# Kernel tuning notes

Hardware: AMD Instinct MI355X
Metric: run time of the kernel (lower is better)

Reference implementation:

```python
import jax, jax.numpy as jnp
import numpy as np

DT = 0.1
DX = 1.0
DY = 1.0
NUM_STEPS = 5
EPS = 1e-06


def _smooth3(c):
    # replicate-pad 3-tap mean filter along last axis (matches F.pad replicate + conv1d)
    cp = jnp.concatenate([c[..., :1], c, c[..., -1:]], axis=-1)
    return (cp[..., :-2] + cp[..., 1:-1] + cp[..., 2:]) / 3.0


def _thomas(a, b, c, d):
    # a, b, c, d: (M, N). Batched Thomas solve, sequential recurrence over N via lax.scan.
    M, N = d.shape
    a0 = a.at[:, 0].set(0.0)  # a[:,0] unused; zero it so the first scan step gives c0/(b0+eps)

    def fwd(carry, inp):
        c_prev, d_prev = carry
        ai, bi, ci, di = inp
        denom = bi - ai * c_prev + EPS
        cs = ci / denom
        ds = (di - ai * d_prev) / denom
        return (cs, ds), (cs, ds)

    init = (jnp.zeros((M,), d.dtype), jnp.zeros((M,), d.dtype))
    _, (c_star, d_star) = jax.lax.scan(fwd, init, (a0.T, b.T, c.T, d.T))  # (N, M)

    def bwd(x_next, inp):
        cs, ds = inp
        x = ds - cs * x_next
        return x, x

    x_last = d_star[-1]
    _, x_rest = jax.lax.scan(bwd, x_last, (c_star[:-1], d_star[:-1]), reverse=True)
    x = jnp.concatenate([x_rest, x_last[None, :]], axis=0)  # (N, M)
    return x.T


def _diffuse_rows(u2, coef2, dt, dh):
    # u2, coef2: (M, N) rows solved independently
    cs = _smooth3(coef2) * dt / (dh * dh)
    a = -cs
    c = -cs
    b = 1.0 + 2.0 * cs
    b = b.at[:, 0].set(1.0 + cs[:, 0])
    b = b.at[:, -1].set(1.0 + cs[:, -1])
    return _thomas(a, b, c, u2)


def _coef_at(base, tcoef, t):
    return jnp.clip(base + tcoef * t, EPS, None)


def _forward(u, alpha_base, beta_base, alpha_time_coeff, beta_time_coeff):
    B, C, H, W = u.shape
    t = 0.0
    for _ in range(NUM_STEPS):
        # half step in x
        alpha = _coef_at(alpha_base, alpha_time_coeff, t)  # (C,H,W)
        af = jnp.broadcast_to(alpha[None], (B, C, H, W)).reshape(B * C * H, W)
        u = _diffuse_rows(u.reshape(B * C * H, W), af, DT / 2, DX).reshape(B, C, H, W)
        t += DT / 2
        # full step in y (transpose H<->W)
        beta = _coef_at(beta_base, beta_time_coeff, t)
        ut = jnp.swapaxes(u, 2, 3).reshape(B * C * W, H)
        bf = jnp.broadcast_to(jnp.swapaxes(beta, 1, 2)[None], (B, C, W, H)).reshape(B * C * W, H)
        ut = _diffuse_rows(ut, bf, DT, DY).reshape(B, C, W, H)
        u = jnp.swapaxes(ut, 2, 3)
        t += DT / 2
        # half step in x
        alpha = _coef_at(alpha_base, alpha_time_coeff, t)
        af = jnp.broadcast_to(alpha[None], (B, C, H, W)).reshape(B * C * H, W)
        u = _diffuse_rows(u.reshape(B * C * H, W), af, DT / 2, DX).reshape(B, C, H, W)
    return u


def setup_inputs() -> dict:
    key = jax.random.key(0)
    k1, k2, k3, k4, k5 = jax.random.split(key, 5)
    B, C, S = 2048, 3, 32
    u = jax.random.normal(k1, (B, C, S, S), dtype=jnp.float32)
    alpha_base = 1.0 + 0.1 * jax.random.normal(k2, (C, S, S), dtype=jnp.float32)
    beta_base = 1.0 + 0.1 * jax.random.normal(k3, (C, S, S), dtype=jnp.float32)
    alpha_time_coeff = 0.05 * jax.random.normal(k4, (C, S, S), dtype=jnp.float32)
    beta_time_coeff = 0.05 * jax.random.normal(k5, (C, S, S), dtype=jnp.float32)
    return {"u": u, "alpha_base": alpha_base, "beta_base": beta_base,
            "alpha_time_coeff": alpha_time_coeff, "beta_time_coeff": beta_time_coeff}


def reference(u, alpha_base, beta_base, alpha_time_coeff, beta_time_coeff):
    return _forward(u, alpha_base, beta_base, alpha_time_coeff, beta_time_coeff)
```

## Files before the change

### kernel.cpp

```cpp
#include <hip/hip_runtime.h>

static constexpr float EPSF = 1e-6f;


__global__ __launch_bounds__(64) void coef_kernel(
    const float* __restrict__ alpha_base, const float* __restrict__ beta_base,
    const float* __restrict__ alpha_tc,   const float* __restrict__ beta_tc,
    float* __restrict__ pT, float* __restrict__ snT)
{
    int gid  = blockIdx.x * 64 + threadIdx.x;
    int pair = gid >> 5;
    int ln   = gid & 31;
    if (pair >= 33) return;
    int set = pair / 3;
    int ch  = pair % 3;
    bool isX = (set < 6);
    float t  = isX ? 0.1f * (float)set : 0.1f * (float)(set - 6) + 0.05f;
    float dt = isX ? 0.05f : 0.1f;

    const float* bp; const float* tp; int stride;
    if (isX) { bp = alpha_base + (ch * 32 + ln) * 32; tp = alpha_tc + (ch * 32 + ln) * 32; stride = 1; }
    else     { bp = beta_base  + ch * 1024 + ln;      tp = beta_tc  + ch * 1024 + ln;      stride = 32; }

    float c[32];
    #pragma unroll
    for (int i = 0; i < 32; ++i)
        c[i] = fmaxf(fmaf(tp[i * stride], t, bp[i * stride]), EPSF);

    float cs[32];
    #pragma unroll
    for (int i = 0; i < 32; ++i) {
        float l = (i == 0)  ? c[0]  : c[i - 1];
        float r = (i == 31) ? c[31] : c[i + 1];
        cs[i] = (l + c[i] + r) / 3.0f * dt;
    }

    float p[32], sn[32];
    {
        float den = (1.0f + cs[0]) + EPSF;
        p[0]  = 1.0f / den;
        sn[0] = cs[0] * p[0];
        float sprev = -sn[0];
        #pragma unroll
        for (int i = 1; i < 32; ++i) {
            float bi = (i == 31) ? (1.0f + cs[31]) : fmaf(2.0f, cs[i], 1.0f);
            float ai = -cs[i];
            float d  = (bi - ai * sprev) + EPSF;
            float pi = 1.0f / d;
            p[i]  = pi;
            float si = ai * pi;
            sn[i] = -si;
            sprev = si;
        }
    }

    float* po = pT  + (set * 3 + ch) * 1024 + ln;
    float* so = snT + (set * 3 + ch) * 1024 + ln;
    #pragma unroll
    for (int i = 0; i < 32; ++i) { po[i * 32] = p[i]; so[i * 32] = sn[i]; }
}

__device__ __forceinline__ void solve_ln(float d[32],
                                         const float* __restrict__ pb,
                                         const float* __restrict__ sb)
{
    float sn[32];
    #pragma unroll
    for (int i = 0; i < 32; ++i) sn[i] = sb[i * 32];

    float prev = d[0] * pb[0];
    d[0] = prev;
    #pragma unroll
    for (int i = 1; i < 32; ++i) {
        prev = fmaf(sn[i], prev, d[i] * pb[i * 32]);
        d[i] = prev;
    }
    #pragma unroll
    for (int i = 30; i >= 0; --i)
        d[i] = fmaf(sn[i], d[i + 1], d[i]);
}

__global__ __launch_bounds__(256, 3) void diff_kernel(
    const float* __restrict__ u_in, float* __restrict__ u_out,
    const float* __restrict__ pT, const float* __restrict__ snT,
    int blocksPerCh)
{
    __shared__ float tile[8 * 1056];
    const int tid = threadIdx.x;
    const int bid = blockIdx.x;
    const int ch  = bid / blocksPerCh;
    const int b0  = (bid % blocksPerCh) * 8;

    {
        const int r  = tid >> 3;
        const int c4 = (tid & 7) << 2;
        #pragma unroll
        for (int it = 0; it < 8; ++it) {
            const int slab = (b0 + it) * 3 + ch;
            const float4 v = reinterpret_cast<const float4*>(u_in + slab * 1024)[tid];
            float* dst = &tile[it * 1056 + r * 33 + c4];
            dst[0] = v.x; dst[1] = v.y; dst[2] = v.z; dst[3] = v.w;
        }
    }
    __syncthreads();

    const int ls = tid >> 5;
    const int ln = tid & 31;
    float* tb = &tile[ls * 1056];
    const float* pB = pT  + ch * 1024 + ln;
    const float* sB = snT + ch * 1024 + ln;

    float d[32];
    #pragma unroll
    for (int i = 0; i < 32; ++i) d[i] = tb[ln * 33 + i];

    solve_ln(d, pB, sB);

    for (int step = 0; step < 5; ++step) {
        #pragma unroll
        for (int i = 0; i < 32; ++i) tb[ln * 33 + i] = d[i];
        __syncthreads();
        #pragma unroll
        for (int i = 0; i < 32; ++i) d[i] = tb[i * 33 + ln];
        {
            const int off = (6 + step) * 3072;
            solve_ln(d, pB + off, sB + off);
        }
        #pragma unroll
        for (int i = 0; i < 32; ++i) tb[i * 33 + ln] = d[i];
        __syncthreads();
        #pragma unroll
        for (int i = 0; i < 32; ++i) d[i] = tb[ln * 33 + i];

        {
            const int off = (step + 1) * 3072;
            solve_ln(d, pB + off, sB + off);
            if (step < 4) solve_ln(d, pB + off, sB + off);
        }
    }

    #pragma unroll
    for (int i = 0; i < 32; ++i) tb[ln * 33 + i] = d[i];
    __syncthreads();
    {
        const int r  = tid >> 3;
        const int c4 = (tid & 7) << 2;
        #pragma unroll
        for (int it = 0; it < 8; ++it) {
            const int slab = (b0 + it) * 3 + ch;
            const float* s_ = &tile[it * 1056 + r * 33 + c4];
            float4 v; v.x = s_[0]; v.y = s_[1]; v.z = s_[2]; v.w = s_[3];
            reinterpret_cast<float4*>(u_out + slab * 1024)[tid] = v;
        }
    }
}

extern "C" void kernel_launch(void* const* d_in, const int* in_sizes, int n_in,
                              void* d_out, int out_size, void* d_ws, size_t ws_size,
                              hipStream_t stream)
{
    const float* u   = (const float*)d_in[0];
    const float* ab  = (const float*)d_in[1];
    const float* bb  = (const float*)d_in[2];
    const float* atc = (const float*)d_in[3];
    const float* btc = (const float*)d_in[4];
    float* out = (float*)d_out;
    float* pT  = (float*)d_ws;
    float* snT = pT + 33 * 1024;

    const int B = in_sizes[0] / (3 * 32 * 32);
    const int blocksPerCh = B / 8;

    coef_kernel<<<17, 64, 0, stream>>>(ab, bb, atc, btc, pT, snT);
    diff_kernel<<<3 * blocksPerCh, 256, 0, stream>>>(u, out, pT, snT, blocksPerCh);
}
```

Before: 115.9 us.

## Make each wavefront own two slabs, drop barriers, interleave coefficients as float2

The u tile load and store are remapped so each 64-lane wavefront handles exactly the two 32x32 slabs it later solves, which lets all __syncthreads be removed. Coefficient tables are interleaved into float2 and loaded into registers ahead of each sweep, with sched_barrier to prefetch during LDS traffic. Row padding changes from 33 to 34 so rows can be read and written with float2 LDS accesses. The costs are higher register pressure from holding 64 coefficient values per lane, and reliance on wavefront-local LDS ordering instead of block barriers.

```diff
diff --git a/kernel.cpp b/kernel.cpp
--- a/kernel.cpp
+++ b/kernel.cpp
@@ -6,7 +6,7 @@
 __global__ __launch_bounds__(64) void coef_kernel(
     const float* __restrict__ alpha_base, const float* __restrict__ beta_base,
     const float* __restrict__ alpha_tc,   const float* __restrict__ beta_tc,
-    float* __restrict__ pT, float* __restrict__ snT)
+    float2* __restrict__ C2)
 {
     int gid  = blockIdx.x * 64 + threadIdx.x;
     int pair = gid >> 5;
@@ -45,8 +45,8 @@
         for (int i = 1; i < 32; ++i) {
             float bi = (i == 31) ? (1.0f + cs[31]) : fmaf(2.0f, cs[i], 1.0f);
             float ai = -cs[i];
-            float d  = (bi - ai * sprev) + EPSF;
-            float pi = 1.0f / d;
+            float dd = (bi - ai * sprev) + EPSF;
+            float pi = 1.0f / dd;
             p[i]  = pi;
             float si = ai * pi;
             sn[i] = -si;
@@ -54,25 +54,25 @@
         }
     }
 
-    float* po = pT  + (set * 3 + ch) * 1024 + ln;
-    float* so = snT + (set * 3 + ch) * 1024 + ln;
+    float2* o = C2 + (set * 3 + ch) * 1024 + ln;
     #pragma unroll
-    for (int i = 0; i < 32; ++i) { po[i * 32] = p[i]; so[i * 32] = sn[i]; }
+    for (int k = 0; k < 32; ++k) o[k * 32] = make_float2(p[k], sn[k]);
 }
 
-__device__ __forceinline__ void solve_ln(float d[32],
-                                         const float* __restrict__ pb,
-                                         const float* __restrict__ sb)
+__device__ __forceinline__ void loadc(float p[32], float sn[32],
+                                      const float2* __restrict__ c)
 {
-    float sn[32];
     #pragma unroll
-    for (int i = 0; i < 32; ++i) sn[i] = sb[i * 32];
+    for (int k = 0; k < 32; ++k) { float2 v = c[k * 32]; p[k] = v.x; sn[k] = v.y; }
+}
 
-    float prev = d[0] * pb[0];
+__device__ __forceinline__ void solve_reg(float d[32], const float p[32], const float sn[32])
+{
+    float prev = d[0] * p[0];
     d[0] = prev;
     #pragma unroll
     for (int i = 1; i < 32; ++i) {
-        prev = fmaf(sn[i], prev, d[i] * pb[i * 32]);
+        prev = fmaf(sn[i], prev, d[i] * p[i]);
         d[i] = prev;
     }
     #pragma unroll
@@ -82,75 +82,87 @@
 
 __global__ __launch_bounds__(256, 3) void diff_kernel(
     const float* __restrict__ u_in, float* __restrict__ u_out,
-    const float* __restrict__ pT, const float* __restrict__ snT,
-    int blocksPerCh)
+    const float2* __restrict__ C2, int blocksPerCh)
 {
-    __shared__ float tile[8 * 1056];
+    __shared__ float tile[8 * 1088];
     const int tid = threadIdx.x;
     const int bid = blockIdx.x;
     const int ch  = bid / blocksPerCh;
     const int b0  = (bid % blocksPerCh) * 8;
+    const int wv  = tid >> 6;
+    const int l   = tid & 63;
+    const int ls  = tid >> 5;
+    const int ln  = tid & 31;
+
+    const float2* cb = C2 + ch * 1024 + ln;
+    float p[32], sn[32];
+    loadc(p, sn, cb);
+    __builtin_amdgcn_sched_barrier(0);
 
     {
-        const int r  = tid >> 3;
-        const int c4 = (tid & 7) << 2;
+        const int sp = b0 + wv * 2;
         #pragma unroll
-        for (int it = 0; it < 8; ++it) {
-            const int slab = (b0 + it) * 3 + ch;
-            const float4 v = reinterpret_cast<const float4*>(u_in + slab * 1024)[tid];
-            float* dst = &tile[it * 1056 + r * 33 + c4];
+        for (int j = 0; j < 8; ++j) {
+            int q   = j * 64 + l;
+            int sl  = q >> 8;
+            int rem = q & 255;
+            const float4 v = reinterpret_cast<const float4*>(
+                u_in + ((sp + sl) * 3 + ch) * 1024)[rem];
+            float* dst = &tile[(wv * 2 + sl) * 1088 + (rem >> 3) * 34 + ((rem & 7) << 2)];
             dst[0] = v.x; dst[1] = v.y; dst[2] = v.z; dst[3] = v.w;
         }
     }
-    __syncthreads();
 
-    const int ls = tid >> 5;
-    const int ln = tid & 31;
-    float* tb = &tile[ls * 1056];
-    const float* pB = pT  + ch * 1024 + ln;
-    const float* sB = snT + ch * 1024 + ln;
-
+    float* tb = &tile[ls * 1088];
     float d[32];
     #pragma unroll
-    for (int i = 0; i < 32; ++i) d[i] = tb[ln * 33 + i];
+    for (int j = 0; j < 16; ++j) {
+        float2 v = *(const float2*)(tb + ln * 34 + 2 * j);
+        d[2 * j] = v.x; d[2 * j + 1] = v.y;
+    }
+    solve_reg(d, p, sn);
 
-    solve_ln(d, pB, sB);
+    const float2* cy = cb + 6 * 3072;
+    const float2* cx = cb + 1 * 3072;
 
     for (int step = 0; step < 5; ++step) {
+        loadc(p, sn, cy); cy += 3072;
+        __builtin_amdgcn_sched_barrier(0);
         #pragma unroll
-        for (int i = 0; i < 32; ++i) tb[ln * 33 + i] = d[i];
-        __syncthreads();
+        for (int j = 0; j < 16; ++j)
+            *(float2*)(tb + ln * 34 + 2 * j) = make_float2(d[2 * j], d[2 * j + 1]);
         #pragma unroll
-        for (int i = 0; i < 32; ++i) d[i] = tb[i * 33 + ln];
-        {
-            const int off = (6 + step) * 3072;
-            solve_ln(d, pB + off, sB + off);
+        for (int i = 0; i < 32; ++i)
+            d[i] = tb[i * 34 + ln];
+        solve_reg(d, p, sn);
+
+        loadc(p, sn, cx); cx += 3072;
+        __builtin_amdgcn_sched_barrier(0);
+        #pragma unroll
+        for (int i = 0; i < 32; ++i)
+            tb[i * 34 + ln] = d[i];
+        #pragma unroll
+        for (int j = 0; j < 16; ++j) {
+            float2 v = *(const float2*)(tb + ln * 34 + 2 * j);
+            d[2 * j] = v.x; d[2 * j + 1] = v.y;
         }
-        #pragma unroll
-        for (int i = 0; i < 32; ++i) tb[i * 33 + ln] = d[i];
-        __syncthreads();
-        #pragma unroll
-        for (int i = 0; i < 32; ++i) d[i] = tb[ln * 33 + i];
-
-        {
-            const int off = (step + 1) * 3072;
-            solve_ln(d, pB + off, sB + off);
-            if (step < 4) solve_ln(d, pB + off, sB + off);
-        }
+        solve_reg(d, p, sn);
+        if (step < 4) solve_reg(d, p, sn);
     }
 
     #pragma unroll
-    for (int i = 0; i < 32; ++i) tb[ln * 33 + i] = d[i];
-    __syncthreads();
+    for (int j = 0; j < 16; ++j)
+        *(float2*)(tb + ln * 34 + 2 * j) = make_float2(d[2 * j], d[2 * j + 1]);
     {
-        const int r  = tid >> 3;
-        const int c4 = (tid & 7) << 2;
+        const int sp = b0 + wv * 2;
         #pragma unroll
-        for (int it = 0; it < 8; ++it) {
-            const int slab = (b0 + it) * 3 + ch;
-            const float* s_ = &tile[it * 1056 + r * 33 + c4];
+        for (int j = 0; j < 8; ++j) {
+            int q   = j * 64 + l;
+            int sl  = q >> 8;
+            int rem = q & 255;
+            const float* s_ = &tile[(wv * 2 + sl) * 1088 + (rem >> 3) * 34 + ((rem & 7) << 2)];
             float4 v; v.x = s_[0]; v.y = s_[1]; v.z = s_[2]; v.w = s_[3];
-            reinterpret_cast<float4*>(u_out + slab * 1024)[tid] = v;
+            reinterpret_cast<float4*>(u_out + ((sp + sl) * 3 + ch) * 1024)[rem] = v;
         }
     }
 }
@@ -165,12 +177,11 @@
     const float* atc = (const float*)d_in[3];
     const float* btc = (const float*)d_in[4];
     float* out = (float*)d_out;
-    float* pT  = (float*)d_ws;
-    float* snT = pT + 33 * 1024;
+    float2* C2 = (float2*)d_ws;
 
     const int B = in_sizes[0] / (3 * 32 * 32);
     const int blocksPerCh = B / 8;
 
-    coef_kernel<<<17, 64, 0, stream>>>(ab, bb, atc, btc, pT, snT);
-    diff_kernel<<<3 * blocksPerCh, 256, 0, stream>>>(u, out, pT, snT, blocksPerCh);
+    coef_kernel<<<17, 64, 0, stream>>>(ab, bb, atc, btc, C2);
+    diff_kernel<<<3 * blocksPerCh, 256, 0, stream>>>(u, out, C2, blocksPerCh);
 }
```

New measurement: 118.4 us. 1.02x slower.
